# Optimization experiments

Hardware: AMD Instinct MI355X
Metric: run time of the kernel (lower is better)

## Reference

```python
import jax, jax.numpy as jnp
import numpy as np

N = 50000      # nodes
E = 800000     # edges (avg degree 16)
IN = 128       # input feature dim
HID = 32       # per-head hidden dim
OUT = 64       # per-head output dim
H = 2          # heads per layer
NEG = 0.2      # leaky relu negative slope


def setup_inputs() -> dict:
    key = jax.random.key(0)
    ks = jax.random.split(key, 16)
    x = jax.random.normal(ks[0], (N, IN), dtype=jnp.float32)
    src = jax.random.randint(ks[1], (E,), 0, N)
    dst = jax.random.randint(ks[2], (E,), 0, N)

    def lin(k, fin, fout):
        return jax.random.normal(k, (fin, fout), dtype=jnp.float32) * (1.0 / np.sqrt(fin))

    def attn(k, h, d):
        return jax.random.normal(k, (h, d), dtype=jnp.float32) * 0.1

    # layer 0: IN -> H*HID, layer 1: H*HID -> H*HID, layer 2 (output): H*HID -> H*OUT
    W0, al0, ar0, b0 = lin(ks[3], IN, H * HID), attn(ks[4], H, HID), attn(ks[5], H, HID), jnp.zeros((H * HID,), jnp.float32)
    W1, al1, ar1, b1 = lin(ks[6], H * HID, H * HID), attn(ks[7], H, HID), attn(ks[8], H, HID), jnp.zeros((H * HID,), jnp.float32)
    W2, al2, ar2, b2 = lin(ks[9], H * HID, H * OUT), attn(ks[10], H, OUT), attn(ks[11], H, OUT), jnp.zeros((H * OUT,), jnp.float32)
    return {"x": x, "src": src, "dst": dst,
            "W0": W0, "al0": al0, "ar0": ar0, "b0": b0,
            "W1": W1, "al1": al1, "ar1": ar1, "b1": b1,
            "W2": W2, "al2": al2, "ar2": ar2, "b2": b2}


def gat_conv(x, src, dst, W, al, ar, b, heads, out_dim, apply_relu):
    # feat: [N, H, D]
    feat = (x @ W).reshape(-1, heads, out_dim)
    el = jnp.einsum('nhd,hd->nh', feat, al)   # [N, H]
    er = jnp.einsum('nhd,hd->nh', feat, ar)   # [N, H]
    # per-edge attention logits, leaky-relu
    e = jax.nn.leaky_relu(el[src] + er[dst], NEG)          # [E, H]
    # edge softmax over incoming edges of each dst node (numerically stable)
    m = jax.ops.segment_max(e, dst, num_segments=N)        # [N, H]
    m = jnp.where(jnp.isfinite(m), m, 0.0)                 # nodes w/o in-edges
    ex = jnp.exp(e - m[dst])                               # [E, H]
    s = jax.ops.segment_sum(ex, dst, num_segments=N)       # [N, H]
    alpha = ex / s[dst]                                    # [E, H]
    # weighted aggregate of source features into dst nodes
    rst = jax.ops.segment_sum(feat[src] * alpha[:, :, None], dst, num_segments=N)  # [N, H, D]
    rst = rst + b.reshape(1, heads, out_dim)
    if apply_relu:
        rst = jax.nn.relu(rst)
    return rst


def reference(x, src, dst, W0, al0, ar0, b0, W1, al1, ar1, b1, W2, al2, ar2, b2):
    h = gat_conv(x, src, dst, W0, al0, ar0, b0, H, HID, True).reshape(N, H * HID)   # flatten(1)
    h = gat_conv(h, src, dst, W1, al1, ar1, b1, H, HID, True).reshape(N, H * HID)   # flatten(1)
    logits = gat_conv(h, src, dst, W2, al2, ar2, b2, H, OUT, False).mean(axis=1)    # mean over heads -> [N, OUT]
    return logits
```

## Files before the change

kernel.cpp:

```cpp
#include <hip/hip_runtime.h>
#include <hip/hip_bf16.h>
#include <hip/hip_fp16.h>

#define NNODES 50000
#define NEG_SLOPE 0.2f
#define BKT_SHIFT 8
#define NBKT ((NNODES + 255) >> 8)
#define STRIDE 5120
#define PEPT 8

typedef _Float16 half8 __attribute__((ext_vector_type(8)));
typedef float v4f __attribute__((ext_vector_type(4)));

__device__ __forceinline__ int rfl(int v) { return __builtin_amdgcn_readfirstlane(v); }

__device__ __forceinline__ void pack_one(const float* W, _Float16* Wp, int K, int C, int tid) {
    int KC = K / 32;
    int l = tid & 63;
    int kc = (tid >> 6) % KC;
    int t = tid / (KC * 64);
    int cc = l & 15, q = l >> 4;
    half8 b;
#pragma unroll
    for (int j = 0; j < 8; j++)
        b[j] = (_Float16)W[(size_t)(kc * 32 + q * 8 + j) * C + t * 16 + cc];
    *(half8*)(Wp + (size_t)tid * 8) = b;
}

__global__ __launch_bounds__(256) void kernelA(
    const float* __restrict__ x, const float* __restrict__ W0,
    const float* __restrict__ AL, const float* __restrict__ AR,
    _Float16* __restrict__ featA, float2* __restrict__ el2A, float2* __restrict__ er2A,
    int* __restrict__ bcursor,
    const float* __restrict__ W2, _Float16* __restrict__ Wp2, int N) {
    int blk = blockIdx.x;
    if (blk == 782) {
        if (threadIdx.x < NBKT) bcursor[threadIdx.x * 16] = threadIdx.x * STRIDE;
        return;
    }
    if (blk > 782) {
        int tid = (blk - 783) * 256 + threadIdx.x;
        if (tid < 8 * 2 * 64) pack_one(W2, Wp2, 64, 128, tid);
        return;
    }
    int wave = threadIdx.x >> 6, lane = threadIdx.x & 63;
    int mtile = blk * 4 + wave;
    if (mtile * 16 >= N) return;
    int m0 = mtile * 16;
    int c = lane & 15, q = lane >> 4;
    v4f acc[4];
#pragma unroll
    for (int t = 0; t < 4; t++) acc[t] = (v4f){0.f, 0.f, 0.f, 0.f};
    const size_t arow = (size_t)(m0 + c) * 128 + q * 8;
#pragma unroll
    for (int kc = 0; kc < 4; kc++) {
        const float* xr = x + arow + kc * 32;
        float4 f0 = *(const float4*)xr;
        float4 f1 = *(const float4*)(xr + 4);
        float fv[8] = {f0.x, f0.y, f0.z, f0.w, f1.x, f1.y, f1.z, f1.w};
        half8 ah, av;
#pragma unroll
        for (int j = 0; j < 8; j++) {
            ah[j] = (_Float16)fv[j];
            av[j] = (_Float16)(fv[j] - (float)ah[j]);
        }
#pragma unroll
        for (int tt = 0; tt < 4; tt++) {
            half8 b;
#pragma unroll
            for (int j = 0; j < 8; j++)
                b[j] = (_Float16)W0[(size_t)(kc * 32 + q * 8 + j) * 64 + tt * 16 + c];
            acc[tt] = __builtin_amdgcn_mfma_f32_16x16x32_f16(ah, b, acc[tt], 0, 0, 0);
            acc[tt] = __builtin_amdgcn_mfma_f32_16x16x32_f16(av, b, acc[tt], 0, 0, 0);
        }
    }
#pragma unroll
    for (int tt = 0; tt < 4; tt++)
#pragma unroll
        for (int r = 0; r < 4; r++) {
            int row = m0 + q * 4 + r;
            featA[(size_t)row * 64 + tt * 16 + c] = (_Float16)acc[tt][r];
        }
    float alv[4], arv[4];
#pragma unroll
    for (int tt = 0; tt < 4; tt++) { alv[tt] = AL[tt * 16 + c]; arv[tt] = AR[tt * 16 + c]; }
#pragma unroll
    for (int r = 0; r < 4; r++) {
        float l0 = 0.f, l1 = 0.f, r0 = 0.f, r1 = 0.f;
#pragma unroll
        for (int tt = 0; tt < 4; tt++) {
            float v = acc[tt][r];
            if (tt < 2) { l0 = fmaf(v, alv[tt], l0); r0 = fmaf(v, arv[tt], r0); }
            else        { l1 = fmaf(v, alv[tt], l1); r1 = fmaf(v, arv[tt], r1); }
        }
#pragma unroll
        for (int m = 1; m < 16; m <<= 1) {
            l0 += __shfl_xor(l0, m, 64);
            l1 += __shfl_xor(l1, m, 64);
            r0 += __shfl_xor(r0, m, 64);
            r1 += __shfl_xor(r1, m, 64);
        }
        if (c == 0) {
            int row = m0 + q * 4 + r;
            el2A[row] = make_float2(l0, l1);
            er2A[row] = make_float2(r0, r1);
        }
    }
}

__global__ __launch_bounds__(1024) void partition_edges(
    const int* __restrict__ src, const int* __restrict__ dst,
    int* __restrict__ bcursor, int2* __restrict__ ebuf, int E) {
    __shared__ int hist[NBKT];
    __shared__ int gbase[NBKT];
    int t = threadIdx.x;
    for (int i = t; i < NBKT; i += 1024) hist[i] = 0;
    __syncthreads();
    int base = blockIdx.x * 1024 * PEPT;
    int sreg[PEPT], dreg[PEPT], rreg[PEPT], breg[PEPT];
#pragma unroll
    for (int k = 0; k < PEPT; k++) {
        int i = base + k * 1024 + t;
        if (i < E) {
            sreg[k] = src[i];
            dreg[k] = dst[i];
            breg[k] = dreg[k] >> BKT_SHIFT;
            rreg[k] = atomicAdd(&hist[breg[k]], 1);
        } else {
            breg[k] = -1;
        }
    }
    __syncthreads();
    for (int i = t; i < NBKT; i += 1024)
        if (hist[i]) gbase[i] = atomicAdd(&bcursor[i * 16], hist[i]);
    __syncthreads();
#pragma unroll
    for (int k = 0; k < PEPT; k++) {
        if (breg[k] >= 0)
            ebuf[(size_t)(gbase[breg[k]] + rreg[k])] = make_int2(sreg[k], dreg[k]);
    }
}

__global__ __launch_bounds__(256) void local_sort(const int2* __restrict__ ebuf,
                                                  const int* __restrict__ bcursor,
                                                  int2* __restrict__ rowse,
                                                  int* __restrict__ csrc, int N) {
    __shared__ int lcnt[256], lrow[256], ws[4];
    int b = blockIdx.x;
    int d0 = b << BKT_SHIFT;
    int t = threadIdx.x;
    int base = b * STRIDE;
    int endE = bcursor[b * 16];
    lcnt[t] = 0;
    __syncthreads();
    for (int i = base + t; i < endE; i += 256)
        atomicAdd(&lcnt[ebuf[i].y - d0], 1);
    __syncthreads();
    int v = lcnt[t];
    int lane = t & 63;
    int x = v;
#pragma unroll
    for (int m = 1; m < 64; m <<= 1) {
        int y = __shfl_up(x, m, 64);
        if (lane >= m) x += y;
    }
    if (lane == 63) ws[t >> 6] = x;
    __syncthreads();
    int w = t >> 6, waveoff = 0;
#pragma unroll
    for (int k = 0; k < 4; k++) if (k < w) waveoff += ws[k];
    int excl = base + waveoff + x - v;
    lrow[t] = excl;
    int d = d0 + t;
    if (d < N) rowse[d] = make_int2(excl, excl + v);
    lcnt[t] = 0;
    __syncthreads();
    for (int i = base + t; i < endE; i += 256) {
        int2 e = ebuf[i];
        int ld = e.y - d0;
        int p = lrow[ld] + atomicAdd(&lcnt[ld], 1);
        csrc[p] = e.x;
    }
}

__global__ __launch_bounds__(256) void agg0_gemm1(
    const int2* __restrict__ rowse, const int* __restrict__ csrc,
    const float2* __restrict__ el2A, const float2* __restrict__ er2A,
    const _Float16* __restrict__ featA, const float* __restrict__ b0,
    const float* __restrict__ W1, const float* __restrict__ al1, const float* __restrict__ ar1,
    _Float16* __restrict__ featB, float2* __restrict__ el2B, float2* __restrict__ er2B,
    int N) {
    __shared__ int2 stA[4][64], stB[4][64];
    __shared__ float vbuf[4][64];
    int wave = threadIdx.x >> 6, lane = threadIdx.x & 63, h = lane >> 5;
    float bl = b0[lane];
    float w1r[64];
#pragma unroll
    for (int k = 0; k < 64; k++) w1r[k] = W1[k * 64 + lane];
    float al1v = al1[lane], ar1v = ar1[lane];
    const int2* stH = h ? stB[wave] : stA[wave];
    for (int n0 = blockIdx.x * 4 + wave; n0 < N; n0 += gridDim.x * 4) {
        int n = rfl(n0);
        int2 se = rowse[n];
        int beg = rfl(se.x), end = rfl(se.y);
        float2 rr = er2A[n];
        float s = 0.f, acc = 0.f;
        for (int base = beg; base < end; base += 64) {
            int idx = base + lane;
            int sv = 0; float wxv = 0.f, wyv = 0.f;
            if (idx < end) {
                sv = csrc[idx];
                float2 l = el2A[sv];
                float t0 = l.x + rr.x; t0 = t0 > 0.f ? t0 : NEG_SLOPE * t0;
                float t1 = l.y + rr.y; t1 = t1 > 0.f ? t1 : NEG_SLOPE * t1;
                wxv = __expf(t0); wyv = __expf(t1);
            }
            stA[wave][lane] = make_int2(sv, __float_as_int(wxv));
            stB[wave][lane] = make_int2(sv, __float_as_int(wyv));
            int cnt = min(64, end - base);
            int j = 0;
            for (; j + 7 < cnt; j += 8) {
                int4 e01 = *(const int4*)(stH + j);
                int4 e23 = *(const int4*)(stH + j + 2);
                int4 e45 = *(const int4*)(stH + j + 4);
                int4 e67 = *(const int4*)(stH + j + 6);
                float f0 = (float)featA[(size_t)e01.x * 64 + lane];
                float f1 = (float)featA[(size_t)e01.z * 64 + lane];
                float f2 = (float)featA[(size_t)e23.x * 64 + lane];
                float f3 = (float)featA[(size_t)e23.z * 64 + lane];
                float f4 = (float)featA[(size_t)e45.x * 64 + lane];
                float f5 = (float)featA[(size_t)e45.z * 64 + lane];
                float f6 = (float)featA[(size_t)e67.x * 64 + lane];
                float f7 = (float)featA[(size_t)e67.z * 64 + lane];
                float w0 = __int_as_float(e01.y), w1 = __int_as_float(e01.w);
                float w2 = __int_as_float(e23.y), w3 = __int_as_float(e23.w);
                float w4 = __int_as_float(e45.y), w5 = __int_as_float(e45.w);
                float w6 = __int_as_float(e67.y), w7 = __int_as_float(e67.w);
                s += ((w0 + w1) + (w2 + w3)) + ((w4 + w5) + (w6 + w7));
                acc = fmaf(w0, f0, acc);
                acc = fmaf(w1, f1, acc);
                acc = fmaf(w2, f2, acc);
                acc = fmaf(w3, f3, acc);
                acc = fmaf(w4, f4, acc);
                acc = fmaf(w5, f5, acc);
                acc = fmaf(w6, f6, acc);
                acc = fmaf(w7, f7, acc);
            }
            for (; j < cnt; j++) {
                int2 e = stH[j];
                float w0 = __int_as_float(e.y);
                float f0 = (float)featA[(size_t)e.x * 64 + lane];
                s += w0;
                acc = fmaf(w0, f0, acc);
            }
        }
        float v = (s > 0.f) ? acc / s : 0.f;
        v = fmaxf(v + bl, 0.f);
        vbuf[wave][lane] = v;
        const float4* vv = (const float4*)vbuf[wave];
        float f = 0.f;
#pragma unroll
        for (int kk = 0; kk < 16; kk++) {
            float4 v4 = vv[kk];
            f = fmaf(v4.x, w1r[4 * kk + 0], f);
            f = fmaf(v4.y, w1r[4 * kk + 1], f);
            f = fmaf(v4.z, w1r[4 * kk + 2], f);
            f = fmaf(v4.w, w1r[4 * kk + 3], f);
        }
        featB[(size_t)n * 64 + lane] = (_Float16)f;
        float vl = f * al1v, vr = f * ar1v;
#pragma unroll
        for (int m = 1; m < 32; m <<= 1) {
            vl += __shfl_xor(vl, m, 64);
            vr += __shfl_xor(vr, m, 64);
        }
        if ((lane & 31) == 0) {
            ((float*)el2B)[n * 2 + h] = vl;
            ((float*)er2B)[n * 2 + h] = vr;
        }
    }
}

__global__ __launch_bounds__(256) void aggregate32(
    const int2* __restrict__ rowse, const int* __restrict__ csrc,
    const float2* __restrict__ el2, const float2* __restrict__ er2,
    const _Float16* __restrict__ feat16, const float* __restrict__ b,
    _Float16* __restrict__ ahi, _Float16* __restrict__ alo, int N) {
    __shared__ int2 stA[4][64], stB[4][64];
    int wave = threadIdx.x >> 6, lane = threadIdx.x & 63, h = lane >> 5;
    int n = rfl(blockIdx.x * 4 + wave);
    if (n >= N) return;
    float bl = b[lane];
    int2 se = rowse[n];
    int beg = rfl(se.x), end = rfl(se.y);
    float2 rr = er2[n];
    const int2* stH = h ? stB[wave] : stA[wave];
    float s = 0.f, acc = 0.f;
    for (int base = beg; base < end; base += 64) {
        int idx = base + lane;
        int sv = 0; float wxv = 0.f, wyv = 0.f;
        if (idx < end) {
            sv = csrc[idx];
            float2 l = el2[sv];
            float t0 = l.x + rr.x; t0 = t0 > 0.f ? t0 : NEG_SLOPE * t0;
            float t1 = l.y + rr.y; t1 = t1 > 0.f ? t1 : NEG_SLOPE * t1;
            wxv = __expf(t0); wyv = __expf(t1);
        }
        stA[wave][lane] = make_int2(sv, __float_as_int(wxv));
        stB[wave][lane] = make_int2(sv, __float_as_int(wyv));
        int cnt = min(64, end - base);
        int j = 0;
        for (; j + 7 < cnt; j += 8) {
            int4 e01 = *(const int4*)(stH + j);
            int4 e23 = *(const int4*)(stH + j + 2);
            int4 e45 = *(const int4*)(stH + j + 4);
            int4 e67 = *(const int4*)(stH + j + 6);
            float f0 = (float)feat16[(size_t)e01.x * 64 + lane];
            float f1 = (float)feat16[(size_t)e01.z * 64 + lane];
            float f2 = (float)feat16[(size_t)e23.x * 64 + lane];
            float f3 = (float)feat16[(size_t)e23.z * 64 + lane];
            float f4 = (float)feat16[(size_t)e45.x * 64 + lane];
            float f5 = (float)feat16[(size_t)e45.z * 64 + lane];
            float f6 = (float)feat16[(size_t)e67.x * 64 + lane];
            float f7 = (float)feat16[(size_t)e67.z * 64 + lane];
            float w0 = __int_as_float(e01.y), w1 = __int_as_float(e01.w);
            float w2 = __int_as_float(e23.y), w3 = __int_as_float(e23.w);
            float w4 = __int_as_float(e45.y), w5 = __int_as_float(e45.w);
            float w6 = __int_as_float(e67.y), w7 = __int_as_float(e67.w);
            s += ((w0 + w1) + (w2 + w3)) + ((w4 + w5) + (w6 + w7));
            acc = fmaf(w0, f0, acc);
            acc = fmaf(w1, f1, acc);
            acc = fmaf(w2, f2, acc);
            acc = fmaf(w3, f3, acc);
            acc = fmaf(w4, f4, acc);
            acc = fmaf(w5, f5, acc);
            acc = fmaf(w6, f6, acc);
            acc = fmaf(w7, f7, acc);
        }
        for (; j < cnt; j++) {
            int2 e = stH[j];
            float w0 = __int_as_float(e.y);
            float f0 = (float)feat16[(size_t)e.x * 64 + lane];
            s += w0;
            acc = fmaf(w0, f0, acc);
        }
    }
    float v = (s > 0.f) ? acc / s : 0.f;
    v = fmaxf(v + bl, 0.f);
    _Float16 hv = (_Float16)v;
    ahi[(size_t)n * 64 + lane] = hv;
    alo[(size_t)n * 64 + lane] = (_Float16)(v - (float)hv);
}

__global__ __launch_bounds__(256) void gemm_mfma2(
    const _Float16* __restrict__ Ahi, const _Float16* __restrict__ Alo,
    const _Float16* __restrict__ Wp,
    const float* __restrict__ AL, const float* __restrict__ AR,
    __half2* __restrict__ feat2, float2* __restrict__ el2, float2* __restrict__ er2,
    int N) {
    constexpr int KC = 2, NT = 8;
    int wave = threadIdx.x >> 6, lane = threadIdx.x & 63;
    int mtile = blockIdx.x * 4 + wave;
    if (mtile * 16 >= N) return;
    int m0 = mtile * 16;
    int c = lane & 15, q = lane >> 4;
    v4f acc[NT];
#pragma unroll
    for (int t = 0; t < NT; t++) acc[t] = (v4f){0.f, 0.f, 0.f, 0.f};
    const size_t arow = (size_t)(m0 + c) * 64 + q * 8;
#pragma unroll
    for (int kc = 0; kc < KC; kc++) {
        half8 ah = *(const half8*)(Ahi + arow + kc * 32);
        half8 av = *(const half8*)(Alo + arow + kc * 32);
#pragma unroll
        for (int t = 0; t < NT; t++) {
            half8 b = *(const half8*)(Wp + ((size_t)(t * KC + kc) * 64 + lane) * 8);
            acc[t] = __builtin_amdgcn_mfma_f32_16x16x32_f16(ah, b, acc[t], 0, 0, 0);
            acc[t] = __builtin_amdgcn_mfma_f32_16x16x32_f16(av, b, acc[t], 0, 0, 0);
        }
    }
#pragma unroll
    for (int t = 0; t < NT / 2; t++)
#pragma unroll
        for (int r = 0; r < 4; r++) {
            int row = m0 + q * 4 + r;
            feat2[(size_t)row * 64 + t * 16 + c] =
                __floats2half2_rn(acc[t][r], acc[t + NT / 2][r]);
        }
    float alv[NT], arv[NT];
#pragma unroll
    for (int t = 0; t < NT; t++) { alv[t] = AL[t * 16 + c]; arv[t] = AR[t * 16 + c]; }
#pragma unroll
    for (int r = 0; r < 4; r++) {
        float l0 = 0.f, l1 = 0.f, r0 = 0.f, r1 = 0.f;
#pragma unroll
        for (int t = 0; t < NT; t++) {
            float v = acc[t][r];
            if (t < NT / 2) { l0 = fmaf(v, alv[t], l0); r0 = fmaf(v, arv[t], r0); }
            else            { l1 = fmaf(v, alv[t], l1); r1 = fmaf(v, arv[t], r1); }
        }
#pragma unroll
        for (int m = 1; m < 16; m <<= 1) {
            l0 += __shfl_xor(l0, m, 64);
            l1 += __shfl_xor(l1, m, 64);
            r0 += __shfl_xor(r0, m, 64);
            r1 += __shfl_xor(r1, m, 64);
        }
        if (c == 0) {
            int row = m0 + q * 4 + r;
            el2[row] = make_float2(l0, l1);
            er2[row] = make_float2(r0, r1);
        }
    }
}

__global__ __launch_bounds__(256) void aggregate64_mean(
    const int2* __restrict__ rowse, const int* __restrict__ csrc,
    const float2* __restrict__ el2, const float2* __restrict__ er2,
    const __half2* __restrict__ feat2, const float* __restrict__ b,
    float* __restrict__ out, int N) {
    __shared__ int4 st[4][64];
    int wave = threadIdx.x >> 6, lane = threadIdx.x & 63;
    int n = rfl(blockIdx.x * 4 + wave);
    if (n >= N) return;
    float b0 = b[lane], b1 = b[64 + lane];
    int2 se = rowse[n];
    int beg = rfl(se.x), end = rfl(se.y);
    float2 rr = er2[n];
    float s0 = 0.f, s1 = 0.f, a0 = 0.f, a1 = 0.f;
    for (int base = beg; base < end; base += 64) {
        int idx = base + lane;
        int sv = 0; float wxv = 0.f, wyv = 0.f;
        if (idx < end) {
            sv = csrc[idx];
            float2 l = el2[sv];
            float t0 = l.x + rr.x; t0 = t0 > 0.f ? t0 : NEG_SLOPE * t0;
            float t1 = l.y + rr.y; t1 = t1 > 0.f ? t1 : NEG_SLOPE * t1;
            wxv = __expf(t0); wyv = __expf(t1);
        }
        st[wave][lane] = make_int4(sv, __float_as_int(wxv), __float_as_int(wyv), 0);
        int cnt = min(64, end - base);
        int j = 0;
        for (; j + 7 < cnt; j += 8) {
            float2 fv[8]; float wxs[8], wys[8];
#pragma unroll
            for (int u = 0; u < 8; u++) {
                int4 e = st[wave][j + u];
                wxs[u] = __int_as_float(e.y);
                wys[u] = __int_as_float(e.z);
                fv[u] = __half22float2(feat2[(size_t)e.x * 64 + lane]);
            }
#pragma unroll
            for (int u = 0; u < 8; u++) {
                s0 += wxs[u]; s1 += wys[u];
                a0 = fmaf(wxs[u], fv[u].x, a0);
                a1 = fmaf(wys[u], fv[u].y, a1);
            }
        }
        for (; j < cnt; j++) {
            int4 e = st[wave][j];
            float wx0 = __int_as_float(e.y), wy0 = __int_as_float(e.z);
            float2 f0 = __half22float2(feat2[(size_t)e.x * 64 + lane]);
            s0 += wx0; s1 += wy0;
            a0 = fmaf(wx0, f0.x, a0); a1 = fmaf(wy0, f0.y, a1);
        }
    }
    float v0 = (s0 > 0.f) ? a0 / s0 : 0.f;
    float v1 = (s1 > 0.f) ? a1 / s1 : 0.f;
    out[(size_t)n * 64 + lane] = 0.5f * ((v0 + b0) + (v1 + b1));
}


extern "C" void kernel_launch(void* const* d_in, const int* in_sizes, int n_in,
                              void* d_out, int out_size, void* d_ws, size_t ws_size,
                              hipStream_t stream) {
    const float* x   = (const float*)d_in[0];
    const int*   src = (const int*)d_in[1];
    const int*   dst = (const int*)d_in[2];
    const float* W0  = (const float*)d_in[3];
    const float* al0 = (const float*)d_in[4];
    const float* ar0 = (const float*)d_in[5];
    const float* b0  = (const float*)d_in[6];
    const float* W1  = (const float*)d_in[7];
    const float* al1 = (const float*)d_in[8];
    const float* ar1 = (const float*)d_in[9];
    const float* b1  = (const float*)d_in[10];
    const float* W2  = (const float*)d_in[11];
    const float* al2 = (const float*)d_in[12];
    const float* ar2 = (const float*)d_in[13];
    const float* b2  = (const float*)d_in[14];
    float* out = (float*)d_out;

    const int N = NNODES;
    const int E = in_sizes[1];

    char* p = (char*)d_ws;
    auto alloc = [&](size_t bytes) {
        void* r = (void*)p;
        p += (bytes + 255) & ~(size_t)255;
        return r;
    };
    int*    bcursor = (int*)alloc((size_t)NBKT * 16 * 4);
    int2*   rowse   = (int2*)alloc((size_t)N * 8);
    int2*   ebuf    = (int2*)alloc(((size_t)NBKT * STRIDE + 4096) * 8);
    int*    csrc    = (int*)alloc(((size_t)NBKT * STRIDE + 4096) * 4);
    float2* el2A    = (float2*)alloc((size_t)N * 8);
    float2* er2A    = (float2*)alloc((size_t)N * 8);
    float2* el2B    = (float2*)alloc((size_t)N * 8);
    float2* er2B    = (float2*)alloc((size_t)N * 8);
    _Float16* ahi   = (_Float16*)alloc((size_t)N * 64 * 2);
    _Float16* alo   = (_Float16*)alloc((size_t)N * 64 * 2);
    void*   featA   = alloc((size_t)N * 64 * 4);
    _Float16* featB = (_Float16*)alloc((size_t)N * 64 * 2);
    _Float16* Wp2   = (_Float16*)alloc(8 * 2 * 64 * 8 * 2);

    kernelA<<<787, 256, 0, stream>>>(x, W0, al0, ar0, (_Float16*)featA, el2A, er2A,
                                     bcursor, W2, Wp2, N);
    int pb = (E + 1024 * PEPT - 1) / (1024 * PEPT);
    partition_edges<<<pb, 1024, 0, stream>>>(src, dst, bcursor, ebuf, E);
    local_sort<<<NBKT, 256, 0, stream>>>(ebuf, bcursor, rowse, csrc, N);

    int nb4 = (N + 3) / 4;
    agg0_gemm1<<<2048, 256, 0, stream>>>(rowse, csrc, el2A, er2A, (const _Float16*)featA,
                                         b0, W1, al1, ar1, featB, el2B, er2B, N);
    aggregate32<<<nb4, 256, 0, stream>>>(rowse, csrc, el2B, er2B, featB, b1, ahi, alo, N);
    int gb = (N / 16 + 3) / 4;
    gemm_mfma2<<<gb, 256, 0, stream>>>(ahi, alo, Wp2, al2, ar2, (__half2*)featA, el2A, er2A, N);
    aggregate64_mean<<<nb4, 256, 0, stream>>>(rowse, csrc, el2A, er2A, (const __half2*)featA,
                                              b2, out, N);
}
```

Before: 246.2 us.

## Fuse layer-1 aggregation with layer-2 GEMM in a persistent per-node kernel

Merges aggregate32 and the MFMA gemm_mfma2 into one persistent kernel (agg1_gemm2). Each wave aggregates a node, stages the 64-wide result in shared memory, then multiplies by W2 held transposed in LDS using scalar FMAs, and computes el/er with wave-wide reductions. This drops one launch and the write and re-read of the hi/lo split activations, and the W2 packing in kernelA goes away. The cost is a 33KB LDS W2 tile per block and a 64x128 product done on vector FMAs per node instead of MFMA.

Result: slower. 317.9 us (+29.1%).

```diff
diff --git a/kernel.cpp b/kernel.cpp
--- a/kernel.cpp
+++ b/kernel.cpp
@@ -14,33 +14,14 @@
 
 __device__ __forceinline__ int rfl(int v) { return __builtin_amdgcn_readfirstlane(v); }
 
-__device__ __forceinline__ void pack_one(const float* W, _Float16* Wp, int K, int C, int tid) {
-    int KC = K / 32;
-    int l = tid & 63;
-    int kc = (tid >> 6) % KC;
-    int t = tid / (KC * 64);
-    int cc = l & 15, q = l >> 4;
-    half8 b;
-#pragma unroll
-    for (int j = 0; j < 8; j++)
-        b[j] = (_Float16)W[(size_t)(kc * 32 + q * 8 + j) * C + t * 16 + cc];
-    *(half8*)(Wp + (size_t)tid * 8) = b;
-}
-
 __global__ __launch_bounds__(256) void kernelA(
     const float* __restrict__ x, const float* __restrict__ W0,
     const float* __restrict__ AL, const float* __restrict__ AR,
     _Float16* __restrict__ featA, float2* __restrict__ el2A, float2* __restrict__ er2A,
-    int* __restrict__ bcursor,
-    const float* __restrict__ W2, _Float16* __restrict__ Wp2, int N) {
+    int* __restrict__ bcursor, int N) {
     int blk = blockIdx.x;
     if (blk == 782) {
         if (threadIdx.x < NBKT) bcursor[threadIdx.x * 16] = threadIdx.x * STRIDE;
-        return;
-    }
-    if (blk > 782) {
-        int tid = (blk - 783) * 256 + threadIdx.x;
-        if (tid < 8 * 2 * 64) pack_one(W2, Wp2, 64, 128, tid);
         return;
     }
     int wave = threadIdx.x >> 6, lane = threadIdx.x & 63;
@@ -281,135 +262,111 @@
     }
 }
 
-__global__ __launch_bounds__(256) void aggregate32(
+__global__ __launch_bounds__(256) void agg1_gemm2(
     const int2* __restrict__ rowse, const int* __restrict__ csrc,
-    const float2* __restrict__ el2, const float2* __restrict__ er2,
-    const _Float16* __restrict__ feat16, const float* __restrict__ b,
-    _Float16* __restrict__ ahi, _Float16* __restrict__ alo, int N) {
+    const float2* __restrict__ el2B, const float2* __restrict__ er2B,
+    const _Float16* __restrict__ featB, const float* __restrict__ b1,
+    const float* __restrict__ W2, const float* __restrict__ al2, const float* __restrict__ ar2,
+    __half2* __restrict__ featC, float2* __restrict__ el2C, float2* __restrict__ er2C,
+    int N) {
     __shared__ int2 stA[4][64], stB[4][64];
+    __shared__ float vbuf[4][64];
+    __shared__ float W2T[128][65];
     int wave = threadIdx.x >> 6, lane = threadIdx.x & 63, h = lane >> 5;
-    int n = rfl(blockIdx.x * 4 + wave);
-    if (n >= N) return;
-    float bl = b[lane];
-    int2 se = rowse[n];
-    int beg = rfl(se.x), end = rfl(se.y);
-    float2 rr = er2[n];
+    for (int idx = threadIdx.x; idx < 8192; idx += 256) {
+        int k = idx >> 7, c = idx & 127;
+        W2T[c][k] = W2[idx];
+    }
+    __syncthreads();
+    float bl = b1[lane];
+    float al2a = al2[lane], al2b = al2[64 + lane];
+    float ar2a = ar2[lane], ar2b = ar2[64 + lane];
     const int2* stH = h ? stB[wave] : stA[wave];
-    float s = 0.f, acc = 0.f;
-    for (int base = beg; base < end; base += 64) {
-        int idx = base + lane;
-        int sv = 0; float wxv = 0.f, wyv = 0.f;
-        if (idx < end) {
-            sv = csrc[idx];
-            float2 l = el2[sv];
-            float t0 = l.x + rr.x; t0 = t0 > 0.f ? t0 : NEG_SLOPE * t0;
-            float t1 = l.y + rr.y; t1 = t1 > 0.f ? t1 : NEG_SLOPE * t1;
-            wxv = __expf(t0); wyv = __expf(t1);
-        }
-        stA[wave][lane] = make_int2(sv, __float_as_int(wxv));
-        stB[wave][lane] = make_int2(sv, __float_as_int(wyv));
-        int cnt = min(64, end - base);
-        int j = 0;
-        for (; j + 7 < cnt; j += 8) {
-            int4 e01 = *(const int4*)(stH + j);
-            int4 e23 = *(const int4*)(stH + j + 2);
-            int4 e45 = *(const int4*)(stH + j + 4);
-            int4 e67 = *(const int4*)(stH + j + 6);
-            float f0 = (float)feat16[(size_t)e01.x * 64 + lane];
-            float f1 = (float)feat16[(size_t)e01.z * 64 + lane];
-            float f2 = (float)feat16[(size_t)e23.x * 64 + lane];
-            float f3 = (float)feat16[(size_t)e23.z * 64 + lane];
-            float f4 = (float)feat16[(size_t)e45.x * 64 + lane];
-            float f5 = (float)feat16[(size_t)e45.z * 64 + lane];
-            float f6 = (float)feat16[(size_t)e67.x * 64 + lane];
-            float f7 = (float)feat16[(size_t)e67.z * 64 + lane];
-            float w0 = __int_as_float(e01.y), w1 = __int_as_float(e01.w);
-            float w2 = __int_as_float(e23.y), w3 = __int_as_float(e23.w);
-            float w4 = __int_as_float(e45.y), w5 = __int_as_float(e45.w);
-            float w6 = __int_as_float(e67.y), w7 = __int_as_float(e67.w);
-            s += ((w0 + w1) + (w2 + w3)) + ((w4 + w5) + (w6 + w7));
-            acc = fmaf(w0, f0, acc);
-            acc = fmaf(w1, f1, acc);
-            acc = fmaf(w2, f2, acc);
-            acc = fmaf(w3, f3, acc);
-            acc = fmaf(w4, f4, acc);
-            acc = fmaf(w5, f5, acc);
-            acc = fmaf(w6, f6, acc);
-            acc = fmaf(w7, f7, acc);
-        }
-        for (; j < cnt; j++) {
-            int2 e = stH[j];
-            float w0 = __int_as_float(e.y);
-            float f0 = (float)feat16[(size_t)e.x * 64 + lane];
-            s += w0;
-            acc = fmaf(w0, f0, acc);
-        }
-    }
-    float v = (s > 0.f) ? acc / s : 0.f;
-    v = fmaxf(v + bl, 0.f);
-    _Float16 hv = (_Float16)v;
-    ahi[(size_t)n * 64 + lane] = hv;
-    alo[(size_t)n * 64 + lane] = (_Float16)(v - (float)hv);
-}
-
-__global__ __launch_bounds__(256) void gemm_mfma2(
-    const _Float16* __restrict__ Ahi, const _Float16* __restrict__ Alo,
-    const _Float16* __restrict__ Wp,
-    const float* __restrict__ AL, const float* __restrict__ AR,
-    __half2* __restrict__ feat2, float2* __restrict__ el2, float2* __restrict__ er2,
-    int N) {
-    constexpr int KC = 2, NT = 8;
-    int wave = threadIdx.x >> 6, lane = threadIdx.x & 63;
-    int mtile = blockIdx.x * 4 + wave;
-    if (mtile * 16 >= N) return;
-    int m0 = mtile * 16;
-    int c = lane & 15, q = lane >> 4;
-    v4f acc[NT];
-#pragma unroll
-    for (int t = 0; t < NT; t++) acc[t] = (v4f){0.f, 0.f, 0.f, 0.f};
-    const size_t arow = (size_t)(m0 + c) * 64 + q * 8;
-#pragma unroll
-    for (int kc = 0; kc < KC; kc++) {
-        half8 ah = *(const half8*)(Ahi + arow + kc * 32);
-        half8 av = *(const half8*)(Alo + arow + kc * 32);
-#pragma unroll
-        for (int t = 0; t < NT; t++) {
-            half8 b = *(const half8*)(Wp + ((size_t)(t * KC + kc) * 64 + lane) * 8);
-            acc[t] = __builtin_amdgcn_mfma_f32_16x16x32_f16(ah, b, acc[t], 0, 0, 0);
-            acc[t] = __builtin_amdgcn_mfma_f32_16x16x32_f16(av, b, acc[t], 0, 0, 0);
-        }
-    }
-#pragma unroll
-    for (int t = 0; t < NT / 2; t++)
-#pragma unroll
-        for (int r = 0; r < 4; r++) {
-            int row = m0 + q * 4 + r;
-            feat2[(size_t)row * 64 + t * 16 + c] =
-                __floats2half2_rn(acc[t][r], acc[t + NT / 2][r]);
-        }
-    float alv[NT], arv[NT];
-#pragma unroll
-    for (int t = 0; t < NT; t++) { alv[t] = AL[t * 16 + c]; arv[t] = AR[t * 16 + c]; }
-#pragma unroll
-    for (int r = 0; r < 4; r++) {
-        float l0 = 0.f, l1 = 0.f, r0 = 0.f, r1 = 0.f;
-#pragma unroll
-        for (int t = 0; t < NT; t++) {
-            float v = acc[t][r];
-            if (t < NT / 2) { l0 = fmaf(v, alv[t], l0); r0 = fmaf(v, arv[t], r0); }
-            else            { l1 = fmaf(v, alv[t], l1); r1 = fmaf(v, arv[t], r1); }
-        }
-#pragma unroll
-        for (int m = 1; m < 16; m <<= 1) {
+    for (int n0 = blockIdx.x * 4 + wave; n0 < N; n0 += gridDim.x * 4) {
+        int n = rfl(n0);
+        int2 se = rowse[n];
+        int beg = rfl(se.x), end = rfl(se.y);
+        float2 rr = er2B[n];
+        float s = 0.f, acc = 0.f;
+        for (int base = beg; base < end; base += 64) {
+            int idx = base + lane;
+            int sv = 0; float wxv = 0.f, wyv = 0.f;
+            if (idx < end) {
+                sv = csrc[idx];
+                float2 l = el2B[sv];
+                float t0 = l.x + rr.x; t0 = t0 > 0.f ? t0 : NEG_SLOPE * t0;
+                float t1 = l.y + rr.y; t1 = t1 > 0.f ? t1 : NEG_SLOPE * t1;
+                wxv = __expf(t0); wyv = __expf(t1);
+            }
+            stA[wave][lane] = make_int2(sv, __float_as_int(wxv));
+            stB[wave][lane] = make_int2(sv, __float_as_int(wyv));
+            int cnt = min(64, end - base);
+            int j = 0;
+            for (; j + 7 < cnt; j += 8) {
+                int4 e01 = *(const int4*)(stH + j);
+                int4 e23 = *(const int4*)(stH + j + 2);
+                int4 e45 = *(const int4*)(stH + j + 4);
+                int4 e67 = *(const int4*)(stH + j + 6);
+                float f0 = (float)featB[(size_t)e01.x * 64 + lane];
+                float f1 = (float)featB[(size_t)e01.z * 64 + lane];
+                float f2 = (float)featB[(size_t)e23.x * 64 + lane];
+                float f3 = (float)featB[(size_t)e23.z * 64 + lane];
+                float f4 = (float)featB[(size_t)e45.x * 64 + lane];
+                float f5 = (float)featB[(size_t)e45.z * 64 + lane];
+                float f6 = (float)featB[(size_t)e67.x * 64 + lane];
+                float f7 = (float)featB[(size_t)e67.z * 64 + lane];
+                float w0 = __int_as_float(e01.y), w1 = __int_as_float(e01.w);
+                float w2 = __int_as_float(e23.y), w3 = __int_as_float(e23.w);
+                float w4 = __int_as_float(e45.y), w5 = __int_as_float(e45.w);
+                float w6 = __int_as_float(e67.y), w7 = __int_as_float(e67.w);
+                s += ((w0 + w1) + (w2 + w3)) + ((w4 + w5) + (w6 + w7));
+                acc = fmaf(w0, f0, acc);
+                acc = fmaf(w1, f1, acc);
+                acc = fmaf(w2, f2, acc);
+                acc = fmaf(w3, f3, acc);
+                acc = fmaf(w4, f4, acc);
+                acc = fmaf(w5, f5, acc);
+                acc = fmaf(w6, f6, acc);
+                acc = fmaf(w7, f7, acc);
+            }
+            for (; j < cnt; j++) {
+                int2 e = stH[j];
+                float w0 = __int_as_float(e.y);
+                float f0 = (float)featB[(size_t)e.x * 64 + lane];
+                s += w0;
+                acc = fmaf(w0, f0, acc);
+            }
+        }
+        float v = (s > 0.f) ? acc / s : 0.f;
+        v = fmaxf(v + bl, 0.f);
+        vbuf[wave][lane] = v;
+        const float4* vv = (const float4*)vbuf[wave];
+        const float4* w0r = (const float4*)&W2T[lane][0];
+        const float4* w1r = (const float4*)&W2T[64 + lane][0];
+        float f0 = 0.f, f1 = 0.f;
+#pragma unroll
+        for (int kk = 0; kk < 16; kk++) {
+            float4 vq = vv[kk];
+            float4 a4 = w0r[kk];
+            float4 b4 = w1r[kk];
+            f0 = fmaf(vq.x, a4.x, f0); f1 = fmaf(vq.x, b4.x, f1);
+            f0 = fmaf(vq.y, a4.y, f0); f1 = fmaf(vq.y, b4.y, f1);
+            f0 = fmaf(vq.z, a4.z, f0); f1 = fmaf(vq.z, b4.z, f1);
+            f0 = fmaf(vq.w, a4.w, f0); f1 = fmaf(vq.w, b4.w, f1);
+        }
+        featC[(size_t)n * 64 + lane] = __floats2half2_rn(f0, f1);
+        float l0 = f0 * al2a, l1 = f1 * al2b;
+        float r0 = f0 * ar2a, r1 = f1 * ar2b;
+#pragma unroll
+        for (int m = 1; m < 64; m <<= 1) {
             l0 += __shfl_xor(l0, m, 64);
             l1 += __shfl_xor(l1, m, 64);
             r0 += __shfl_xor(r0, m, 64);
             r1 += __shfl_xor(r1, m, 64);
         }
-        if (c == 0) {
-            int row = m0 + q * 4 + r;
-            el2[row] = make_float2(l0, l1);
-            er2[row] = make_float2(r0, r1);
+        if (lane == 0) {
+            el2C[n] = make_float2(l0, l1);
+            er2C[n] = make_float2(r0, r1);
         }
     }
 }
@@ -508,24 +465,21 @@
     float2* er2A    = (float2*)alloc((size_t)N * 8);
     float2* el2B    = (float2*)alloc((size_t)N * 8);
     float2* er2B    = (float2*)alloc((size_t)N * 8);
-    _Float16* ahi   = (_Float16*)alloc((size_t)N * 64 * 2);
-    _Float16* alo   = (_Float16*)alloc((size_t)N * 64 * 2);
     void*   featA   = alloc((size_t)N * 64 * 4);
     _Float16* featB = (_Float16*)alloc((size_t)N * 64 * 2);
-    _Float16* Wp2   = (_Float16*)alloc(8 * 2 * 64 * 8 * 2);
-
-    kernelA<<<787, 256, 0, stream>>>(x, W0, al0, ar0, (_Float16*)featA, el2A, er2A,
-                                     bcursor, W2, Wp2, N);
+
+    _Float16* fA  = (_Float16*)featA;
+    __half2*  fC  = (__half2*)featA;
+
+    kernelA<<<783, 256, 0, stream>>>(x, W0, al0, ar0, fA, el2A, er2A, bcursor, N);
     int pb = (E + 1024 * PEPT - 1) / (1024 * PEPT);
     partition_edges<<<pb, 1024, 0, stream>>>(src, dst, bcursor, ebuf, E);
     local_sort<<<NBKT, 256, 0, stream>>>(ebuf, bcursor, rowse, csrc, N);
 
     int nb4 = (N + 3) / 4;
-    agg0_gemm1<<<2048, 256, 0, stream>>>(rowse, csrc, el2A, er2A, (const _Float16*)featA,
+    agg0_gemm1<<<2048, 256, 0, stream>>>(rowse, csrc, el2A, er2A, fA,
                                          b0, W1, al1, ar1, featB, el2B, er2B, N);
-    aggregate32<<<nb4, 256, 0, stream>>>(rowse, csrc, el2B, er2B, featB, b1, ahi, alo, N);
-    int gb = (N / 16 + 3) / 4;
-    gemm_mfma2<<<gb, 256, 0, stream>>>(ahi, alo, Wp2, al2, ar2, (__half2*)featA, el2A, er2A, N);
-    aggregate64_mean<<<nb4, 256, 0, stream>>>(rowse, csrc, el2A, er2A, (const __half2*)featA,
-                                              b2, out, N);
-}
+    agg1_gemm2<<<2048, 256, 0, stream>>>(rowse, csrc, el2B, er2B, featB,
+                                         b1, W2, al2, ar2, fC, el2A, er2A, N);
+    aggregate64_mean<<<nb4, 256, 0, stream>>>(rowse, csrc, el2A, er2A, fC, b2, out, N);
+}
```
